# Kernel tuning notes

Measured on AMD Instinct MI355X. Metric: run time of the kernel, lower is better.

Reference implementation:

```python
import jax, jax.numpy as jnp
import numpy as np

NUM_HEADS = 12
DIM = 768


def setup_inputs() -> dict:
    key = jax.random.key(0)
    ks = jax.random.split(key, 7)
    B, S, E = 8, 1024, DIM
    s = 0.02
    return {
        "x": jax.random.normal(ks[0], (B, S, E), dtype=jnp.float32),
        "Wq": jax.random.normal(ks[1], (E, E), dtype=jnp.float32) * s,
        "bq": jnp.zeros((E,), dtype=jnp.float32),
        "Wk": jax.random.normal(ks[2], (E, E), dtype=jnp.float32) * s,
        "bk": jnp.zeros((E,), dtype=jnp.float32),
        "Wo": jax.random.normal(ks[3], (E, E), dtype=jnp.float32) * s,
        "bo": jnp.zeros((E,), dtype=jnp.float32),
    }


def reference(x, Wq, bq, Wk, bk, Wo, bo):
    B, S, E = x.shape
    n = NUM_HEADS
    d = E // n
    scale = d ** (-0.5)

    def heads(t):  # [B,S,E] -> [B,n,S,d]
        return t.reshape(B, S, n, d).transpose(0, 2, 1, 3)

    q = heads(x @ Wq.T + bq)
    k = heads(x @ Wk.T + bk)
    v = k  # faithful to source bug: v = self.k_w(x)

    attn = jnp.einsum('bnqd,bnkd->bnqk', q, k) * scale  # [B,n,S,S]
    attn = jax.nn.softmax(attn, axis=-1)
    out = jnp.einsum('bnqk,bnkd->bnqd', attn, v)  # [B,n,S,d]
    out = out.transpose(0, 2, 1, 3).reshape(B, S, E)
    return out @ Wo.T + bo
```

## Files before the change

### kernel.cpp

```cpp
#include <hip/hip_runtime.h>
#include <stdint.h>


using short8   = __attribute__((ext_vector_type(8))) short;
using uint4v   = __attribute__((ext_vector_type(4))) unsigned;
using float4v  = __attribute__((ext_vector_type(4))) float;
using float16v = __attribute__((ext_vector_type(16))) float;

struct __align__(8) U2 { unsigned x, y; };

__device__ __forceinline__ void async16(void* lds, const void* g) {
  __builtin_amdgcn_global_load_lds(
      (const __attribute__((address_space(1))) void*)g,
      (__attribute__((address_space(3))) void*)lds, 16, 0, 0);
}

#define LGKM_WAIT  asm volatile("s_waitcnt lgkmcnt(0)" ::: "memory")
#define BARRIER    asm volatile("s_barrier" ::: "memory")

template <int N> __device__ __forceinline__ void vm_wait() {
  if constexpr (N == 4) asm volatile("s_waitcnt vmcnt(4)" ::: "memory");
  else if constexpr (N == 0) asm volatile("s_waitcnt vmcnt(0)" ::: "memory");
}

__device__ __forceinline__ unsigned bf16b(float f) {
  union { float f; unsigned u; } v; v.f = f;
  unsigned r = v.u + 0x7FFFu + ((v.u >> 16) & 1u);
  return r >> 16;
}
__device__ __forceinline__ unsigned rne_adj(float f) {
  union { float f; unsigned u; } v; v.f = f;
  return v.u + 0x7FFFu + ((v.u >> 16) & 1u);
}
__device__ __forceinline__ unsigned pack_hi16(unsigned a, unsigned b) {
  return __builtin_amdgcn_perm(a, b, 0x07060302u);
}

__global__ __launch_bounds__(256) void cvt_bf16(const float* __restrict__ in,
                                                unsigned short* __restrict__ out,
                                                int n8) {
  int i = blockIdx.x * 256 + threadIdx.x;
  if (i >= n8) return;
  const float4v* p = (const float4v*)in;
  float4v a = p[i * 2], b = p[i * 2 + 1];
  uint4v w;
  w[0] = pack_hi16(rne_adj(a[1]), rne_adj(a[0]));
  w[1] = pack_hi16(rne_adj(a[3]), rne_adj(a[2]));
  w[2] = pack_hi16(rne_adj(b[1]), rne_adj(b[0]));
  w[3] = pack_hi16(rne_adj(b[3]), rne_adj(b[2]));
  ((uint4v*)out)[i] = w;
}

__global__ __launch_bounds__(256) void cvt_w3(const float* __restrict__ w0,
                                              const float* __restrict__ w1,
                                              const float* __restrict__ w2,
                                              unsigned short* __restrict__ o0,
                                              unsigned short* __restrict__ o1,
                                              unsigned short* __restrict__ o2) {
  int mi = blockIdx.x / 288;
  int i = (blockIdx.x - mi * 288) * 256 + threadIdx.x;
  const float* in = (mi == 0) ? w0 : (mi == 1) ? w1 : w2;
  unsigned short* out = (mi == 0) ? o0 : (mi == 1) ? o1 : o2;
  const float4v* p = (const float4v*)in;
  float4v a = p[i * 2], b = p[i * 2 + 1];
  uint4v w;
  w[0] = pack_hi16(rne_adj(a[1]), rne_adj(a[0]));
  w[1] = pack_hi16(rne_adj(a[3]), rne_adj(a[2]));
  w[2] = pack_hi16(rne_adj(b[1]), rne_adj(b[0]));
  w[3] = pack_hi16(rne_adj(b[3]), rne_adj(b[2]));
  ((uint4v*)out)[i] = w;
}

template <int BUF, int WAIT, class F1, class F2, class F3, class F4>
__device__ __forceinline__ void ktile4(const char* lds, int aoff, int boff,
                                       float4v (&acc)[2][2][2][4],
                                       F1&& s1, F2&& s2, F3&& s3, F4&& s4) {
  constexpr int AB = BUF * 65536;
  constexpr int BB = BUF * 65536 + 32768;
  short8 af[2][2], b0[4][2], b1[4][2];

#define RD_A(MH)                                                              \
  _Pragma("unroll") for (int mf = 0; mf < 2; ++mf)                            \
  _Pragma("unroll") for (int ks = 0; ks < 2; ++ks)                            \
    af[mf][ks] = *(const short8*)(lds + AB + (MH)*16384 + aoff + mf*2048 + ks*64);
#define RD_B(NH, BF)                                                          \
  _Pragma("unroll") for (int nf = 0; nf < 4; ++nf)                            \
  _Pragma("unroll") for (int ks = 0; ks < 2; ++ks)                            \
    BF[nf][ks] = *(const short8*)(lds + BB + (NH)*16384 + boff + nf*2048 + ks*64);
#define MM(MH, NH, BF)                                                        \
  _Pragma("unroll") for (int mf = 0; mf < 2; ++mf)                            \
  _Pragma("unroll") for (int nf = 0; nf < 4; ++nf)                            \
  _Pragma("unroll") for (int ks = 0; ks < 2; ++ks)                            \
    acc[MH][NH][mf][nf] = __builtin_amdgcn_mfma_f32_16x16x32_bf16(            \
        af[mf][ks], BF[nf][ks], acc[MH][NH][mf][nf], 0, 0, 0);

  RD_A(0) RD_B(0, b0) s1();
  BARRIER; LGKM_WAIT; __builtin_amdgcn_sched_barrier(0);
  __builtin_amdgcn_s_setprio(1); MM(0, 0, b0) __builtin_amdgcn_s_setprio(0);
  BARRIER;
  RD_B(1, b1) s2();
  BARRIER; LGKM_WAIT; __builtin_amdgcn_sched_barrier(0);
  __builtin_amdgcn_s_setprio(1); MM(0, 1, b1) __builtin_amdgcn_s_setprio(0);
  BARRIER;
  RD_A(1) s3();
  BARRIER; LGKM_WAIT; __builtin_amdgcn_sched_barrier(0);
  __builtin_amdgcn_s_setprio(1); MM(1, 1, b1) __builtin_amdgcn_s_setprio(0);
  BARRIER;
  s4();
  BARRIER; LGKM_WAIT; __builtin_amdgcn_sched_barrier(0);
  __builtin_amdgcn_s_setprio(1); MM(1, 0, b0) __builtin_amdgcn_s_setprio(0);
  vm_wait<WAIT>();
  BARRIER;
#undef RD_A
#undef RD_B
#undef MM
}

__global__ __launch_bounds__(512, 2) void sgemm_qk8(
    const unsigned short* __restrict__ A, const unsigned short* __restrict__ B,
    const float* __restrict__ bias0, const float* __restrict__ bias1,
    unsigned short* __restrict__ outq, unsigned short* __restrict__ outk,
    unsigned short* __restrict__ outkt) {
  extern __shared__ __align__(16) char lds[];
  const int tid = threadIdx.x;
  const int w = tid >> 6, lane = tid & 63;
  const int Q4 = lane >> 4, r = lane & 15;
  const int wr = w & 3, wc = w >> 2;
  const int bid = blockIdx.x;
  const int wg = (bid & 7) * 24 + (bid >> 3);
  const int m0 = (wg / 6) * 256;
  const int n0 = (wg % 6) * 256;

  const int srow = lane >> 3;
  const int scol = ((lane & 7) * 8) ^ ((lane >> 5) * 16);

  auto stA = [&](int buf, int half, int t) {
#pragma unroll
    for (int j = 0; j < 2; ++j)
      async16(lds + buf * 65536 + half * 16384 + (w * 2 + j) * 1024 + lane * 16,
              A + (size_t)(m0 + half * 128 + (w * 2 + j) * 8 + srow) * 768 +
                  t * 64 + scol);
  };
  auto stB = [&](int buf, int half, int t) {
#pragma unroll
    for (int j = 0; j < 2; ++j)
      async16(lds + buf * 65536 + 32768 + half * 16384 + (w * 2 + j) * 1024 + lane * 16,
              B + (size_t)(n0 + half * 128 + (w * 2 + j) * 8 + srow) * 768 +
                  t * 64 + scol);
  };

  const int flip = ((lane >> 2) & 1) * 32;
  const int aoff = (wr * 32 + r) * 128 + ((Q4 * 16) ^ flip);
  const int boff = (wc * 64 + r) * 128 + ((Q4 * 16) ^ flip);

  float4v acc[2][2][2][4];
#pragma unroll
  for (int a = 0; a < 2; ++a)
#pragma unroll
    for (int b = 0; b < 2; ++b)
#pragma unroll
      for (int c = 0; c < 2; ++c)
#pragma unroll
        for (int d = 0; d < 4; ++d)
#pragma unroll
          for (int g = 0; g < 4; ++g) acc[a][b][c][d][g] = 0.0f;

  stA(0, 0, 0); stB(0, 0, 0); stB(0, 1, 0); stA(0, 1, 0);
  stA(1, 0, 1); stB(1, 1, 1);
  vm_wait<4>(); BARRIER;

#pragma unroll 1
  for (int i = 0; i < 5; ++i) {
    const int t1 = 2 * i + 1, t2 = 2 * i + 2, t3 = 2 * i + 3;
    ktile4<0, 4>(lds, aoff, boff, acc,
                 [&] { stA(1, 1, t1); stB(1, 0, t1); },
                 [&] {},
                 [&] { stA(0, 0, t2); },
                 [&] { stB(0, 1, t2); });
    ktile4<1, 4>(lds, aoff, boff, acc,
                 [&] { stA(0, 1, t2); stB(0, 0, t2); },
                 [&] {},
                 [&] { stA(1, 0, t3); },
                 [&] { stB(1, 1, t3); });
  }
  ktile4<0, 0>(lds, aoff, boff, acc,
               [&] { stA(1, 1, 11); stB(1, 0, 11); },
               [&] {}, [&] {}, [&] {});
  ktile4<1, -1>(lds, aoff, boff, acc, [&] {}, [&] {}, [&] {}, [&] {});

  const bool isq = (n0 < 768);
  const float* bias = isq ? bias0 : bias1;
  unsigned short* outp = isq ? outq : outk;
  const int nb = isq ? n0 : (n0 - 768);
  const float scl = isq ? 0.18033688011112042f : 1.0f;
#pragma unroll
  for (int Nh = 0; Nh < 2; ++Nh)
#pragma unroll
    for (int nf = 0; nf < 4; ++nf) {
      const int n = nb + Nh * 128 + wc * 64 + nf * 16 + r;
      const float bv = bias[n];
#pragma unroll
      for (int Mh = 0; Mh < 2; ++Mh)
#pragma unroll
        for (int mf = 0; mf < 2; ++mf) {
          const int m = m0 + Mh * 128 + wr * 32 + mf * 16 + Q4 * 4;
#pragma unroll
          for (int g = 0; g < 4; ++g)
            outp[(size_t)(m + g) * 768 + n] =
                (unsigned short)bf16b((acc[Mh][Nh][mf][nf][g] + bv) * scl);
        }
    }
  if (!isq) {
    const int bq = m0 >> 10;
    const int sb0 = (m0 & 1023) + wr * 32 + (Q4 & 1) * 8 + (Q4 >> 1) * 4;
#pragma unroll
    for (int Nh = 0; Nh < 2; ++Nh)
#pragma unroll
      for (int nf = 0; nf < 4; ++nf) {
        const int nk = nb + Nh * 128 + wc * 64 + nf * 16 + r;
        const int hh = nk >> 6, dd = nk & 63;
        const float bv = bias1[nk];
#pragma unroll
        for (int Mh = 0; Mh < 2; ++Mh)
#pragma unroll
          for (int mf = 0; mf < 2; ++mf) {
            const int ns = sb0 + Mh * 128 + mf * 16;
            const float4v a4 = acc[Mh][Nh][mf][nf];
            unsigned lo = pack_hi16(rne_adj(a4[1] + bv), rne_adj(a4[0] + bv));
            unsigned hi = pack_hi16(rne_adj(a4[3] + bv), rne_adj(a4[2] + bv));
            *(U2*)(outkt + (size_t)((bq * 12 + hh) * 64 + dd) * 1024 + ns) =
                U2{lo, hi};
          }
      }
  }
}

__global__ __launch_bounds__(256, 3) void sgemm_out(
    const unsigned short* __restrict__ A, const unsigned short* __restrict__ B,
    const float* __restrict__ bias, float* __restrict__ outp) {
  __shared__ __align__(16) unsigned short a_l[4096];
  __shared__ __align__(16) unsigned short b_l[8192];
  const int tid = threadIdx.x;
  const int w = tid >> 6, lane = tid & 63;
  const int Q4 = lane >> 4, r = lane & 15;
  const int m0 = blockIdx.y * 64;
  const int n0 = blockIdx.x * 128;
  const int wm = w >> 1, wn = w & 1;

  float4v acc[2][4];
#pragma unroll
  for (int i = 0; i < 2; ++i)
#pragma unroll
    for (int j = 0; j < 4; ++j)
#pragma unroll
      for (int g = 0; g < 4; ++g) acc[i][j][g] = 0.0f;

  const unsigned short* Ab = A + (size_t)(m0 + r) * 768 + Q4 * 8;
  const unsigned short* Bb = B + (size_t)(n0 + r) * 768 + Q4 * 8;

  uint4v ra[2], rb[4];
  auto gload = [&](int kt) {
#pragma unroll
    for (int ci = 0; ci < 2; ++ci) {
      int idx = w * 2 + ci;
      ra[ci] = *(const uint4v*)(Ab + (idx >> 1) * 12288 + kt + (idx & 1) * 32);
    }
#pragma unroll
    for (int ci = 0; ci < 4; ++ci) {
      int idx = w * 4 + ci;
      rb[ci] = *(const uint4v*)(Bb + (idx >> 1) * 12288 + kt + (idx & 1) * 32);
    }
  };
  auto swrite = [&]() {
#pragma unroll
    for (int ci = 0; ci < 2; ++ci) {
      int idx = w * 2 + ci;
      *(uint4v*)&a_l[idx * 512 + lane * 8] = ra[ci];
    }
#pragma unroll
    for (int ci = 0; ci < 4; ++ci) {
      int idx = w * 4 + ci;
      *(uint4v*)&b_l[idx * 512 + lane * 8] = rb[ci];
    }
  };

  short8 af[2][2], bf[4][2];
  auto loadf = [&]() {
#pragma unroll
    for (int i = 0; i < 2; ++i)
#pragma unroll
      for (int ks = 0; ks < 2; ++ks)
        af[i][ks] = *(const short8*)&a_l[((wm * 2 + i) * 2 + ks) * 512 + lane * 8];
#pragma unroll
    for (int i = 0; i < 4; ++i)
#pragma unroll
      for (int ks = 0; ks < 2; ++ks)
        bf[i][ks] = *(const short8*)&b_l[((wn * 4 + i) * 2 + ks) * 512 + lane * 8];
  };
  auto dot = [&]() {
#pragma unroll
    for (int mt = 0; mt < 2; ++mt)
#pragma unroll
      for (int nt = 0; nt < 4; ++nt)
#pragma unroll
        for (int ks = 0; ks < 2; ++ks)
          acc[mt][nt] = __builtin_amdgcn_mfma_f32_16x16x32_bf16(
              af[mt][ks], bf[nt][ks], acc[mt][nt], 0, 0, 0);
  };

  gload(0);
#pragma unroll 1
  for (int t = 0; t < 12; ++t) {
    if (t > 0) BARRIER;
    swrite();
    if (t < 11) gload(t * 64 + 64);
    LGKM_WAIT;
    BARRIER;
    loadf();
    dot();
  }

#pragma unroll
  for (int nt = 0; nt < 4; ++nt) {
    int n = n0 + wn * 64 + nt * 16 + r;
    float bv = bias[n];
#pragma unroll
    for (int mt = 0; mt < 2; ++mt) {
      int m = m0 + wm * 32 + mt * 16 + Q4 * 4;
#pragma unroll
      for (int g = 0; g < 4; ++g)
        outp[(size_t)(m + g) * 768 + n] = acc[mt][nt][g] + bv;
    }
  }
}

__global__ __launch_bounds__(256, 3) void attn_fused(
    const unsigned short* __restrict__ qg,
    const unsigned short* __restrict__ kg,
    const unsigned short* __restrict__ ktg,
    unsigned short* __restrict__ ao) {
  __shared__ __align__(16) unsigned short q_l[8192];
  __shared__ __align__(16) unsigned short k_l[8192];
  __shared__ __align__(16) unsigned short vt_l[8192];

  const int tid = threadIdx.x;
  const int w = tid >> 6, lane = tid & 63;
  const int l31 = lane & 31, hi = lane >> 5;
  const int bid = blockIdx.x;
  const int b = bid & 7;
  const int h = bid >> 6;
  const int qt = (bid >> 3) & 7;
  const int q0 = qt * 128;
  const int bh = b * 12 + h;

#pragma unroll
  for (int ci = 0; ci < 4; ++ci) {
    int c = w * 4 + ci;
    async16(&q_l[c * 512 + lane * 8],
            qg + ((size_t)(b * 1024 + q0 + (c >> 2) * 32 + l31) * 768 + h * 64 + (c & 3) * 16 + hi * 8));
    async16(&k_l[c * 512 + lane * 8],
            kg + ((size_t)(b * 1024 + (c >> 2) * 32 + l31) * 768 + h * 64 + (c & 3) * 16 + hi * 8));
    async16(&vt_l[c * 512 + lane * 8],
            ktg + ((size_t)(bh * 64 + (c >> 3) * 32 + l31) * 1024 + (c & 7) * 16 + hi * 8));
  }
  __syncthreads();

  short8 bfq[4];
#pragma unroll
  for (int kb = 0; kb < 4; ++kb)
    bfq[kb] = *(const short8*)&q_l[(w * 4 + kb) * 512 + lane * 8];

  float16v o_acc[2];
#pragma unroll
  for (int db = 0; db < 2; ++db)
#pragma unroll
    for (int e = 0; e < 16; ++e) o_acc[db][e] = 0.0f;
  float ps = 0.0f;

#pragma unroll 1
  for (int it = 0; it < 8; ++it) {
    float16v sc[4];
#pragma unroll
    for (int sb = 0; sb < 4; ++sb)
#pragma unroll
      for (int e = 0; e < 16; ++e) sc[sb][e] = 0.0f;
    __builtin_amdgcn_s_setprio(1);
#pragma unroll
    for (int sb = 0; sb < 4; ++sb)
#pragma unroll
      for (int kb = 0; kb < 4; ++kb) {
        short8 af = *(const short8*)&k_l[(sb * 4 + kb) * 512 + lane * 8];
        sc[sb] = __builtin_amdgcn_mfma_f32_32x32x16_bf16(af, bfq[kb], sc[sb], 0, 0, 0);
      }
    __builtin_amdgcn_s_setprio(0);

    BARRIER;
    if (it < 7) {
      const int s1 = (it + 1) * 128;
#pragma unroll
      for (int ci = 0; ci < 4; ++ci) {
        int c = w * 4 + ci;
        async16(&k_l[c * 512 + lane * 8],
                kg + ((size_t)(b * 1024 + s1 + (c >> 2) * 32 + l31) * 768 + h * 64 + (c & 3) * 16 + hi * 8));
      }
      vm_wait<4>();
    } else {
      vm_wait<0>();
    }
    BARRIER;

#pragma unroll
    for (int sb = 0; sb < 4; ++sb) {
      float pe[16];
#pragma unroll
      for (int e = 0; e < 16; ++e) pe[e] = __builtin_amdgcn_exp2f(sc[sb][e]);
#pragma unroll
      for (int e = 0; e < 16; ++e) ps += pe[e];
      uint4v w0, w1;
#pragma unroll
      for (int p = 0; p < 4; ++p) {
        w0[p] = pack_hi16(rne_adj(pe[2 * p + 1]), rne_adj(pe[2 * p]));
        w1[p] = pack_hi16(rne_adj(pe[2 * p + 9]), rne_adj(pe[2 * p + 8]));
      }
      short8 pf0 = __builtin_bit_cast(short8, w0);
      short8 pf1 = __builtin_bit_cast(short8, w1);
      __builtin_amdgcn_s_setprio(1);
#pragma unroll
      for (int db = 0; db < 2; ++db) {
        short8 vf0 = *(const short8*)&vt_l[(db * 8 + sb * 2) * 512 + lane * 8];
        o_acc[db] = __builtin_amdgcn_mfma_f32_32x32x16_bf16(vf0, pf0, o_acc[db], 0, 0, 0);
        short8 vf1 = *(const short8*)&vt_l[(db * 8 + sb * 2 + 1) * 512 + lane * 8];
        o_acc[db] = __builtin_amdgcn_mfma_f32_32x32x16_bf16(vf1, pf1, o_acc[db], 0, 0, 0);
      }
      __builtin_amdgcn_s_setprio(0);
    }

    if (it < 7) {
      BARRIER;
      const int s1 = (it + 1) * 128;
#pragma unroll
      for (int ci = 0; ci < 4; ++ci) {
        int c = w * 4 + ci;
        async16(&vt_l[c * 512 + lane * 8],
                ktg + ((size_t)(bh * 64 + (c >> 3) * 32 + l31) * 1024 + s1 + (c & 7) * 16 + hi * 8));
      }
      vm_wait<4>();
      BARRIER;
    }
  }

  ps += __shfl_xor(ps, 32, 64);
  const float inv = 1.0f / ps;
  const size_t rowbase = (size_t)(b * 1024 + q0 + w * 32 + l31) * 768 + h * 64;
#pragma unroll
  for (int db = 0; db < 2; ++db)
#pragma unroll
    for (int qq = 0; qq < 4; ++qq) {
      unsigned lo = pack_hi16(rne_adj(o_acc[db][qq * 4 + 1] * inv),
                              rne_adj(o_acc[db][qq * 4 + 0] * inv));
      unsigned hh = pack_hi16(rne_adj(o_acc[db][qq * 4 + 3] * inv),
                              rne_adj(o_acc[db][qq * 4 + 2] * inv));
      *(U2*)(ao + rowbase + db * 32 + qq * 8 + hi * 4) = U2{lo, hh};
    }
}

extern "C" void kernel_launch(void* const* d_in, const int* in_sizes, int n_in,
                              void* d_out, int out_size, void* d_ws, size_t ws_size,
                              hipStream_t stream) {
  const float* x  = (const float*)d_in[0];
  const float* Wq = (const float*)d_in[1];
  const float* bq = (const float*)d_in[2];
  const float* Wk = (const float*)d_in[3];
  const float* bk = (const float*)d_in[4];
  const float* Wo = (const float*)d_in[5];
  const float* bo = (const float*)d_in[6];
  (void)in_sizes; (void)n_in; (void)out_size; (void)ws_size;

  static bool inited = false;
  if (!inited) {
    (void)hipFuncSetAttribute((const void*)sgemm_qk8,
                              hipFuncAttributeMaxDynamicSharedMemorySize, 131072);
    inited = true;
  }

  char* ws = (char*)d_ws;
  unsigned short* x_b   = (unsigned short*)(ws);
  unsigned short* wqk_b = (unsigned short*)(ws + 12582912);
  unsigned short* wo_b  = (unsigned short*)(ws + 14942208);
  unsigned short* q_b   = (unsigned short*)(ws + 16121856);
  unsigned short* k_b   = (unsigned short*)(ws + 28704768);
  unsigned short* kt_b  = (unsigned short*)(ws + 41287680);
  unsigned short* ao_b  = (unsigned short*)(ws + 53870592);

  cvt_bf16<<<3072, 256, 0, stream>>>(x, x_b, 786432);
  cvt_w3<<<864, 256, 0, stream>>>(Wq, Wk, Wo, wqk_b, wqk_b + 589824, wo_b);

  sgemm_qk8<<<192, 512, 131072, stream>>>(x_b, wqk_b, bq, bk, q_b, k_b, kt_b);
  attn_fused<<<768, 256, 0, stream>>>(q_b, k_b, kt_b, ao_b);
  sgemm_out<<<dim3(6, 128), 256, 0, stream>>>(ao_b, wo_b, bo, (float*)d_out);
}
```

Baseline: 192.6 us.

## Software-pipeline attention loop with double-buffered K and QK of next tile

Measured after the change: 340.7 us. +76.9%, slower.

```diff
diff --git a/kernel.cpp b/kernel.cpp
--- a/kernel.cpp
+++ b/kernel.cpp
@@ -339,8 +339,8 @@
     const unsigned short* __restrict__ kg,
     const unsigned short* __restrict__ ktg,
     unsigned short* __restrict__ ao) {
-  __shared__ __align__(16) unsigned short q_l[8192];
-  __shared__ __align__(16) unsigned short k_l[8192];
+  __shared__ __align__(16) unsigned short kb0[8192];
+  __shared__ __align__(16) unsigned short kb1[8192];
   __shared__ __align__(16) unsigned short vt_l[8192];
 
   const int tid = threadIdx.x;
@@ -353,33 +353,46 @@
   const int q0 = qt * 128;
   const int bh = b * 12 + h;
 
+  auto stageK = [&](unsigned short* dst, int s0) {
+#pragma unroll
+    for (int ci = 0; ci < 4; ++ci) {
+      int c = w * 4 + ci;
+      async16(&dst[c * 512 + lane * 8],
+              kg + ((size_t)(b * 1024 + s0 + (c >> 2) * 32 + l31) * 768 + h * 64 + (c & 3) * 16 + hi * 8));
+    }
+  };
+  auto stageV = [&](int s0) {
+#pragma unroll
+    for (int ci = 0; ci < 4; ++ci) {
+      int c = w * 4 + ci;
+      async16(&vt_l[c * 512 + lane * 8],
+              ktg + ((size_t)(bh * 64 + (c >> 3) * 32 + l31) * 1024 + s0 + (c & 7) * 16 + hi * 8));
+    }
+  };
+
 #pragma unroll
   for (int ci = 0; ci < 4; ++ci) {
     int c = w * 4 + ci;
-    async16(&q_l[c * 512 + lane * 8],
+    async16(&kb1[c * 512 + lane * 8],
             qg + ((size_t)(b * 1024 + q0 + (c >> 2) * 32 + l31) * 768 + h * 64 + (c & 3) * 16 + hi * 8));
-    async16(&k_l[c * 512 + lane * 8],
-            kg + ((size_t)(b * 1024 + (c >> 2) * 32 + l31) * 768 + h * 64 + (c & 3) * 16 + hi * 8));
-    async16(&vt_l[c * 512 + lane * 8],
-            ktg + ((size_t)(bh * 64 + (c >> 3) * 32 + l31) * 1024 + (c & 7) * 16 + hi * 8));
-  }
+  }
+  stageK(kb0, 0);
+  stageV(0);
   __syncthreads();
 
   short8 bfq[4];
 #pragma unroll
   for (int kb = 0; kb < 4; ++kb)
-    bfq[kb] = *(const short8*)&q_l[(w * 4 + kb) * 512 + lane * 8];
+    bfq[kb] = *(const short8*)&kb1[(w * 4 + kb) * 512 + lane * 8];
 
   float16v o_acc[2];
 #pragma unroll
   for (int db = 0; db < 2; ++db)
 #pragma unroll
     for (int e = 0; e < 16; ++e) o_acc[db][e] = 0.0f;
-  float ps = 0.0f;
-
-#pragma unroll 1
-  for (int it = 0; it < 8; ++it) {
-    float16v sc[4];
+  float ps0 = 0.0f, ps1 = 0.0f, ps2 = 0.0f, ps3 = 0.0f;
+
+  auto qkc = [&](const unsigned short* kb, float16v (&sc)[4]) {
 #pragma unroll
     for (int sb = 0; sb < 4; ++sb)
 #pragma unroll
@@ -388,67 +401,84 @@
 #pragma unroll
     for (int sb = 0; sb < 4; ++sb)
 #pragma unroll
-      for (int kb = 0; kb < 4; ++kb) {
-        short8 af = *(const short8*)&k_l[(sb * 4 + kb) * 512 + lane * 8];
-        sc[sb] = __builtin_amdgcn_mfma_f32_32x32x16_bf16(af, bfq[kb], sc[sb], 0, 0, 0);
+      for (int kk = 0; kk < 4; ++kk) {
+        short8 af = *(const short8*)&kb[(sb * 4 + kk) * 512 + lane * 8];
+        sc[sb] = __builtin_amdgcn_mfma_f32_32x32x16_bf16(af, bfq[kk], sc[sb], 0, 0, 0);
       }
     __builtin_amdgcn_s_setprio(0);
-
-    BARRIER;
-    if (it < 7) {
-      const int s1 = (it + 1) * 128;
-#pragma unroll
-      for (int ci = 0; ci < 4; ++ci) {
-        int c = w * 4 + ci;
-        async16(&k_l[c * 512 + lane * 8],
-                kg + ((size_t)(b * 1024 + s1 + (c >> 2) * 32 + l31) * 768 + h * 64 + (c & 3) * 16 + hi * 8));
-      }
-      vm_wait<4>();
-    } else {
-      vm_wait<0>();
-    }
-    BARRIER;
-
+  };
+
+  auto expPack = [&](float16v (&sc)[4], short8 (&pf0)[4], short8 (&pf1)[4]) {
 #pragma unroll
     for (int sb = 0; sb < 4; ++sb) {
       float pe[16];
 #pragma unroll
       for (int e = 0; e < 16; ++e) pe[e] = __builtin_amdgcn_exp2f(sc[sb][e]);
 #pragma unroll
-      for (int e = 0; e < 16; ++e) ps += pe[e];
+      for (int e = 0; e < 16; e += 4) {
+        ps0 += pe[e]; ps1 += pe[e + 1]; ps2 += pe[e + 2]; ps3 += pe[e + 3];
+      }
       uint4v w0, w1;
 #pragma unroll
       for (int p = 0; p < 4; ++p) {
         w0[p] = pack_hi16(rne_adj(pe[2 * p + 1]), rne_adj(pe[2 * p]));
         w1[p] = pack_hi16(rne_adj(pe[2 * p + 9]), rne_adj(pe[2 * p + 8]));
       }
-      short8 pf0 = __builtin_bit_cast(short8, w0);
-      short8 pf1 = __builtin_bit_cast(short8, w1);
-      __builtin_amdgcn_s_setprio(1);
+      pf0[sb] = __builtin_bit_cast(short8, w0);
+      pf1[sb] = __builtin_bit_cast(short8, w1);
+    }
+  };
+
+  auto pv = [&](short8 (&pf0)[4], short8 (&pf1)[4]) {
+    __builtin_amdgcn_s_setprio(1);
+#pragma unroll
+    for (int sb = 0; sb < 4; ++sb)
 #pragma unroll
       for (int db = 0; db < 2; ++db) {
         short8 vf0 = *(const short8*)&vt_l[(db * 8 + sb * 2) * 512 + lane * 8];
-        o_acc[db] = __builtin_amdgcn_mfma_f32_32x32x16_bf16(vf0, pf0, o_acc[db], 0, 0, 0);
+        o_acc[db] = __builtin_amdgcn_mfma_f32_32x32x16_bf16(vf0, pf0[sb], o_acc[db], 0, 0, 0);
         short8 vf1 = *(const short8*)&vt_l[(db * 8 + sb * 2 + 1) * 512 + lane * 8];
-        o_acc[db] = __builtin_amdgcn_mfma_f32_32x32x16_bf16(vf1, pf1, o_acc[db], 0, 0, 0);
+        o_acc[db] = __builtin_amdgcn_mfma_f32_32x32x16_bf16(vf1, pf1[sb], o_acc[db], 0, 0, 0);
       }
-      __builtin_amdgcn_s_setprio(0);
-    }
-
-    if (it < 7) {
+    __builtin_amdgcn_s_setprio(0);
+  };
+
+  auto step = [&](int t, float16v (&scIn)[4], float16v (&scOut)[4],
+                  const unsigned short* kNext, unsigned short* kStage) {
+    short8 pf0[4], pf1[4];
+    expPack(scIn, pf0, pf1);
+    if (t < 7) {
+      vm_wait<0>();
       BARRIER;
-      const int s1 = (it + 1) * 128;
-#pragma unroll
-      for (int ci = 0; ci < 4; ++ci) {
-        int c = w * 4 + ci;
-        async16(&vt_l[c * 512 + lane * 8],
-                ktg + ((size_t)(bh * 64 + (c >> 3) * 32 + l31) * 1024 + s1 + (c & 7) * 16 + hi * 8));
+      qkc(kNext, scOut);
+    }
+    pv(pf0, pf1);
+    if (t < 7) {
+      BARRIER;
+      stageV((t + 1) * 128);
+      if (t < 6) {
+        stageK(kStage, (t + 2) * 128);
+        vm_wait<4>();
+      } else {
+        vm_wait<0>();
       }
-      vm_wait<4>();
       BARRIER;
     }
-  }
-
+  };
+
+  float16v scA[4], scB[4];
+  qkc(kb0, scA);
+  LGKM_WAIT;
+  BARRIER;
+  stageK(kb1, 128);
+
+#pragma unroll 1
+  for (int tt = 0; tt < 4; ++tt) {
+    step(2 * tt,     scA, scB, kb1, kb0);
+    step(2 * tt + 1, scB, scA, kb0, kb1);
+  }
+
+  float ps = (ps0 + ps1) + (ps2 + ps3);
   ps += __shfl_xor(ps, 32, 64);
   const float inv = 1.0f / ps;
   const size_t rowbase = (size_t)(b * 1024 + q0 + w * 32 + l31) * 768 + h * 64;
```
